# Kernel optimization log

Hardware: AMD Instinct MI355X
Metric: run time of the kernel (lower is better)

Reference implementation:

```python
import jax, jax.numpy as jnp
import numpy as np

# Graph / model dims (match init_kwargs config)
N1, N2, N3 = 80000, 16000, 4096
E1, E2 = 256000, 65536
D_IN, H1, C1 = 256, 8, 64   # conv1: concat -> 512
H2, C2 = 4, 64              # conv2: mean over heads -> gnn_outdim=64
F_IN, F_HID, L_DIM, N_CLS = 128, 64, 64, 1


def setup_inputs() -> dict:
    key = jax.random.key(0)
    ks = jax.random.split(key, 20)
    rng = np.random.default_rng(0)

    def edges(E, n_src, n_dst):
        src = rng.integers(0, n_src, size=E)
        dst = rng.integers(0, n_dst, size=E)
        # avoid incidental self loops (PyG remove_self_loops); explicit ones added in conv
        src = np.where(src == dst, src + 1, src)
        return jnp.asarray(src, jnp.int32), jnp.asarray(dst, jnp.int32)

    es1, ed1 = edges(E1, N1, N2)
    es2, ed2 = edges(E2, N2, N3)
    s = 0.05
    return {
        "x": jax.random.normal(ks[0], (N1, D_IN), jnp.float32),
        "flat": jax.random.normal(ks[1], (N3, F_IN), jnp.float32),
        "last": jax.random.normal(ks[2], (N3, L_DIM), jnp.float32),
        "edge_src1": es1, "edge_dst1": ed1,
        "edge_src2": es2, "edge_dst2": ed2,
        "W1_src": jax.random.normal(ks[3], (D_IN, H1 * C1), jnp.float32) * s,
        "W1_dst": jax.random.normal(ks[4], (D_IN, H1 * C1), jnp.float32) * s,
        "att1_src": jax.random.normal(ks[5], (H1, C1), jnp.float32) * s,
        "att1_dst": jax.random.normal(ks[6], (H1, C1), jnp.float32) * s,
        "bias1": jax.random.normal(ks[7], (H1 * C1,), jnp.float32) * s,
        "W2_src": jax.random.normal(ks[8], (H1 * C1, H2 * C2), jnp.float32) * s,
        "W2_dst": jax.random.normal(ks[9], (H1 * C1, H2 * C2), jnp.float32) * s,
        "att2_src": jax.random.normal(ks[10], (H2, C2), jnp.float32) * s,
        "att2_dst": jax.random.normal(ks[11], (H2, C2), jnp.float32) * s,
        "bias2": jax.random.normal(ks[12], (C2,), jnp.float32) * s,
        "flat_W": jax.random.normal(ks[13], (F_IN, F_HID), jnp.float32) * s,
        "flat_b": jax.random.normal(ks[14], (F_HID,), jnp.float32) * s,
        "out_W": jax.random.normal(ks[15], (C2 + F_HID + L_DIM, N_CLS), jnp.float32) * s,
        "out_b": jax.random.normal(ks[16], (N_CLS,), jnp.float32) * s,
    }


def gat_conv(x_src, x_dst, src, dst, W_s, W_d, a_s, a_d, b, concat):
    """PyG bipartite GATConv (eval mode, add_self_loops=True, neg slope 0.2)."""
    H, C = a_s.shape
    Ns, Nd = x_src.shape[0], x_dst.shape[0]
    h_s = (x_src @ W_s).reshape(Ns, H, C)
    h_d = (x_dst @ W_d).reshape(Nd, H, C)
    sl = jnp.arange(Nd, dtype=src.dtype)
    src = jnp.concatenate([src, sl])  # self loops on target nodes
    dst = jnp.concatenate([dst, sl])
    e_s = jnp.einsum("nhc,hc->nh", h_s, a_s)  # [Ns,H]
    e_d = jnp.einsum("nhc,hc->nh", h_d, a_d)  # [Nd,H]
    alpha = jax.nn.leaky_relu(e_s[src] + e_d[dst], negative_slope=0.2)  # [E,H]
    amax = jax.ops.segment_max(alpha, dst, num_segments=Nd)[dst]
    ex = jnp.exp(alpha - amax)
    w = ex / jax.ops.segment_sum(ex, dst, num_segments=Nd)[dst]  # segment softmax
    msg = w[:, :, None] * h_s[src]  # [E,H,C]
    out = jax.ops.segment_sum(msg, dst, num_segments=Nd)  # [Nd,H,C]
    out = out.reshape(Nd, H * C) if concat else out.mean(axis=1)
    return out + b


def reference(x, flat, last, edge_src1, edge_dst1, edge_src2, edge_dst2,
              W1_src, W1_dst, att1_src, att1_dst, bias1,
              W2_src, W2_dst, att2_src, att2_dst, bias2,
              flat_W, flat_b, out_W, out_b):
    # eval mode: featdrop / attndrop / main_dropout are identity
    h = gat_conv(x, x[:N2], edge_src1, edge_dst1,
                 W1_src, W1_dst, att1_src, att1_dst, bias1, concat=True)
    h = jax.nn.elu(h)
    h = gat_conv(h, h[:N3], edge_src2, edge_dst2,
                 W2_src, W2_dst, att2_src, att2_dst, bias2, concat=False)
    f = flat @ flat_W + flat_b
    z = jnp.concatenate([h, f, last], axis=1)  # [N3, 64+64+64]
    return z @ out_W + out_b  # [N3, num_cls]
```

## Files before the change

### kernel.cpp

```cpp
#include <hip/hip_runtime.h>
#include <hip/hip_bf16.h>
#include <cstdio>

typedef __attribute__((ext_vector_type(8))) short short8;
typedef __attribute__((ext_vector_type(4))) short short4v;
typedef __attribute__((ext_vector_type(8))) _Float16 half8;
typedef __attribute__((ext_vector_type(4))) float f32x4;

template <int H> struct VecT;
template <> struct VecT<8> { using T = short8; };
template <> struct VecT<4> { using T = short4v; };

__device__ __forceinline__ float bfu2f(unsigned short u) {
    return __uint_as_float(((unsigned)u) << 16);
}
__device__ __forceinline__ unsigned short f2bfu(float f) {
    __hip_bfloat16 b = __float2bfloat16(f);
    union { __hip_bfloat16 b; unsigned short u; } cv; cv.b = b;
    return cv.u;
}
__device__ __forceinline__ unsigned short f2hu(float f) {
    _Float16 h = (_Float16)f;
    union { _Float16 h; unsigned short u; } cv; cv.h = h;
    return cv.u;
}

#define N1 80000
#define N2 16000
#define N3 4096
#define E1 256000
#define E2 65536

__global__ void prep_kernel(const float* __restrict__ W1s, unsigned short* __restrict__ w1s_pk,
                            const float* __restrict__ W2s, unsigned short* __restrict__ w2s_pk,
                            const float* __restrict__ W1d, const float* __restrict__ a1d,
                            float* __restrict__ v1dT,
                            const float* __restrict__ W2d, const float* __restrict__ a2d,
                            float* __restrict__ v2dT,
                            const float* __restrict__ fW, unsigned short* __restrict__ fw_t3,
                            int* __restrict__ zbase, int zn) {
    int i = blockIdx.x * blockDim.x + threadIdx.x;
    const int S0 = 131072, S1 = 131072, S2 = 8192, S3 = 4096;
    if (i < S0) {
        int k = i >> 9, n = i & 511;
        int n16 = n >> 4, l = n & 15, k32 = k >> 5, qq = (k >> 3) & 3, e = k & 7;
        size_t base = ((size_t)(n16 * 8 + k32)) * 512 + (qq * 16 + l) * 8 + e;
        w1s_pk[base] = f2hu(W1s[i]);
    } else if (i < S0 + S1) {
        int j = i - S0;
        int k = j >> 8, n = j & 255;
        int n16 = n >> 4, l = n & 15, k32 = k >> 5, qq = (k >> 3) & 3, e = k & 7;
        size_t base = ((size_t)(n16 * 16 + k32)) * 512 + (qq * 16 + l) * 8 + e;
        w2s_pk[base] = f2hu(W2s[j]);
    } else if (i < S0 + S1 + S2) {
        int j = i - S0 - S1;
        int k = j >> 6, n = j & 63;
        float v = fW[j];
        unsigned short h = f2bfu(v);
        unsigned short l = f2bfu(v - bfu2f(h));
        size_t base = (size_t)n * 384;
        fw_t3[base + k] = h;
        fw_t3[base + 128 + k] = l;
        fw_t3[base + 256 + k] = h;
    } else if (i < S0 + S1 + S2 + S3) {
        int j = i - S0 - S1 - S2;
        if (j < 2048) {
            int h = j >> 8, k = j & 255;
            float s = 0.f;
            for (int c = 0; c < 64; c++) s += W1d[k * 512 + h * 64 + c] * a1d[h * 64 + c];
            v1dT[j] = s;
        } else {
            int jj = j - 2048;
            int h = jj >> 9, k = jj & 511;
            float s = 0.f;
            for (int c = 0; c < 64; c++) s += W2d[k * 256 + h * 64 + c] * a2d[h * 64 + c];
            v2dT[jj] = s;
        }
    } else {
        int j = i - S0 - S1 - S2 - S3;
        if (j < zn) zbase[j] = 0;
    }
}

__global__ void hist_dual(const int* __restrict__ d1, int* __restrict__ c1,
                          const int* __restrict__ d2, int* __restrict__ c2) {
    int i = blockIdx.x * blockDim.x + threadIdx.x;
    if (i < E1) {
        int d = d1[i];
        if ((unsigned)d < (unsigned)N2) atomicAdd(&c1[d], 1);
    } else if (i < E1 + E2) {
        int d = d2[i - E1];
        if ((unsigned)d < (unsigned)N3) atomicAdd(&c2[d], 1);
    }
}
__global__ __launch_bounds__(1024)
void scan_dual(const int* __restrict__ c1, int* __restrict__ s1, int Nd1,
               const int* __restrict__ c2, int* __restrict__ s2, int Nd2) {
    const int* cnt = (blockIdx.x == 0) ? c1 : c2;
    int* start = (blockIdx.x == 0) ? s1 : s2;
    int Nd = (blockIdx.x == 0) ? Nd1 : Nd2;
    __shared__ int part[1024];
    int t = threadIdx.x;
    int k = (Nd + 1023) >> 10;
    int lo = t * k, hi = min(lo + k, Nd);
    if (lo > Nd) lo = Nd;
    int s = 0;
    for (int i = lo; i < hi; i++) s += cnt[i];
    part[t] = s;
    __syncthreads();
    for (int off = 1; off < 1024; off <<= 1) {
        int v = (t >= off) ? part[t - off] : 0;
        __syncthreads();
        part[t] += v;
        __syncthreads();
    }
    int run = (t > 0) ? part[t - 1] : 0;
    for (int i = lo; i < hi; i++) { start[i] = run; run += cnt[i]; }
    if (t == 1023) start[Nd] = part[1023];
}
__global__ void fill_dual(const int* __restrict__ sa1, const int* __restrict__ da1,
                          const int* __restrict__ st1, int* __restrict__ cu1, int* __restrict__ cs1,
                          const int* __restrict__ sa2, const int* __restrict__ da2,
                          const int* __restrict__ st2, int* __restrict__ cu2, int* __restrict__ cs2) {
    int i = blockIdx.x * blockDim.x + threadIdx.x;
    const int *sa, *da, *st;
    int *cu, *cs;
    int Nd, Ns, e;
    if (i < E1) { sa = sa1; da = da1; st = st1; cu = cu1; cs = cs1; Nd = N2; Ns = N1; e = i; }
    else if (i < E1 + E2) { sa = sa2; da = da2; st = st2; cu = cu2; cs = cs2; Nd = N3; Ns = N2; e = i - E1; }
    else return;
    int d = da[e];
    if ((unsigned)d >= (unsigned)Nd) return;
    int p = atomicAdd(&cu[d], 1);
    int idx = st[d] + p;
    if (idx >= st[d + 1]) return;
    int s = sa[e];
    if ((unsigned)s >= (unsigned)Ns) s = 0;
    cs[idx] = s;
}

template <bool AF16>
__global__ __launch_bounds__(256, 2)
void gemm_lds(const void* __restrict__ Ax,
              const unsigned short* __restrict__ Bp, unsigned short* __restrict__ C,
              const float* __restrict__ att, float* __restrict__ es_out,
              int MT, int NB, int N, int K, int H) {
    __shared__ alignas(16) _Float16 As[2][64][72];
    const int hb = blockIdx.x;
    const int xcd = hb & 7;
    const int sI = hb >> 3;
    const int mt = (sI / NB) * 8 + xcd;
    const int nb = sI % NB;
    if (mt >= MT) return;
    const int m0 = mt * 64;
    const int tid = threadIdx.x;
    const int wave = tid >> 6, lane = tid & 63;
    const int q = lane >> 4, l15 = lane & 15;
    const int n0 = nb * 256 + wave * 64;
    const int KS = K >> 6;
    const int KSB = K >> 5;
    const int arow = tid >> 2, ac16 = (tid & 3) * 16;
    const unsigned short* Bbase = Bp + (size_t)(n0 >> 4) * KSB * 512 + lane * 8;

    f32x4 acc[4][4] = {};
    half8 b[2][4];
    float4 s0, s1, s2, s3;
    half8 sh0, sh1;

    auto stageLoad = [&](int t) {
        if constexpr (AF16) {
            const _Float16* p = (const _Float16*)Ax + (size_t)(m0 + arow) * K + t * 64 + ac16;
            sh0 = *(const half8*)p;
            sh1 = *(const half8*)(p + 8);
        } else {
            const float* p = (const float*)Ax + (size_t)(m0 + arow) * K + t * 64 + ac16;
            s0 = *(const float4*)p;
            s1 = *(const float4*)(p + 4);
            s2 = *(const float4*)(p + 8);
            s3 = *(const float4*)(p + 12);
        }
    };
    auto stageWrite = [&](int buf) {
        half8 v0, v1;
        if constexpr (AF16) {
            v0 = sh0; v1 = sh1;
        } else {
            v0[0] = (_Float16)s0.x; v0[1] = (_Float16)s0.y;
            v0[2] = (_Float16)s0.z; v0[3] = (_Float16)s0.w;
            v0[4] = (_Float16)s1.x; v0[5] = (_Float16)s1.y;
            v0[6] = (_Float16)s1.z; v0[7] = (_Float16)s1.w;
            v1[0] = (_Float16)s2.x; v1[1] = (_Float16)s2.y;
            v1[2] = (_Float16)s2.z; v1[3] = (_Float16)s2.w;
            v1[4] = (_Float16)s3.x; v1[5] = (_Float16)s3.y;
            v1[6] = (_Float16)s3.z; v1[7] = (_Float16)s3.w;
        }
        *(half8*)&As[buf][arow][ac16] = v0;
        *(half8*)&As[buf][arow][ac16 + 8] = v1;
    };
    auto loadB = [&](int k32, int kh, int nt) {
        b[kh][nt] = *(const half8*)(Bbase + ((size_t)nt * KSB + k32) * 512);
    };

    stageLoad(0);
#pragma unroll
    for (int kh = 0; kh < 2; kh++)
#pragma unroll
        for (int nt = 0; nt < 4; nt++) loadB(kh, kh, nt);
    stageWrite(0);
    __syncthreads();

    int cur = 0;
    for (int t = 0; t < KS; t++) {
        const bool hn = (t + 1) < KS;
        if (hn) stageLoad(t + 1);
#pragma unroll
        for (int kh = 0; kh < 2; kh++) {
#pragma unroll
            for (int rg = 0; rg < 4; rg++) {
                half8 a = *(const half8*)&As[cur][rg * 16 + l15][kh * 32 + q * 8];
#pragma unroll
                for (int nt = 0; nt < 4; nt++) {
                    acc[rg][nt] = __builtin_amdgcn_mfma_f32_16x16x32_f16(a, b[kh][nt], acc[rg][nt], 0, 0, 0);
                    if (rg == 3 && hn) loadB(2 * (t + 1) + kh, kh, nt);
                }
            }
        }
        if (hn) {
            stageWrite(cur ^ 1);
            __syncthreads();
        }
        cur ^= 1;
    }

#pragma unroll
    for (int rg = 0; rg < 4; rg++)
#pragma unroll
        for (int nt = 0; nt < 4; nt++)
#pragma unroll
            for (int r = 0; r < 4; r++) {
                int row = m0 + rg * 16 + q * 4 + r;
                int col = n0 + nt * 16 + l15;
                C[(size_t)row * N + col] = f2bfu(acc[rg][nt][r]);
            }
    {
        const int head = n0 >> 6;
        float av[4];
#pragma unroll
        for (int nt = 0; nt < 4; nt++) av[nt] = att[head * 64 + nt * 16 + l15];
#pragma unroll
        for (int rg = 0; rg < 4; rg++)
#pragma unroll
            for (int r = 0; r < 4; r++) {
                float p = acc[rg][0][r] * av[0] + acc[rg][1][r] * av[1]
                        + acc[rg][2][r] * av[2] + acc[rg][3][r] * av[3];
#pragma unroll
                for (int off = 1; off < 16; off <<= 1) p += __shfl_xor(p, off);
                if (l15 == 0)
                    es_out[(size_t)(m0 + rg * 16 + q * 4 + r) * H + head] = p;
            }
    }
}

__global__ __launch_bounds__(256)
void gemm_mfma(const float* __restrict__ A, const unsigned short* __restrict__ Bt3,
               float* __restrict__ C, int M, int N, int K) {
    const int KK = 3 * K;
    __shared__ unsigned short As[2][64][72];
    __shared__ unsigned short Bs[64][72];
    const int tid = threadIdx.x;
    const int wave = tid >> 6, lane = tid & 63;
    const int wr = wave >> 1, wc = wave & 1;
    const int quad = lane >> 4, l15 = lane & 15;
    const int m0 = blockIdx.y * 64, n0 = blockIdx.x * 64;
    f32x4 acc[2][2] = {};
    for (int k0 = 0; k0 < KK; k0 += 64) {
        const int seg = k0 / K;
        const int ks = k0 - seg * K;
#pragma unroll
        for (int i = 0; i < 2; i++) {
            int idx = tid + i * 256;
            int r = idx >> 3, cv = (idx & 7) * 8;
            const float* ap = &A[(size_t)(m0 + r) * K + ks + cv];
            const float4 v0 = *(const float4*)ap;
            const float4 v1 = *(const float4*)(ap + 4);
            float va[8] = {v0.x, v0.y, v0.z, v0.w, v1.x, v1.y, v1.z, v1.w};
            short8 h8, l8;
#pragma unroll
            for (int j = 0; j < 8; j++) {
                unsigned short hh = f2bfu(va[j]);
                h8[j] = (short)hh;
                l8[j] = (short)f2bfu(va[j] - bfu2f(hh));
            }
            *(short8*)&As[0][r][cv] = h8;
            *(short8*)&As[1][r][cv] = l8;
            *(short8*)&Bs[r][cv] = *(const short8*)&Bt3[(size_t)(n0 + r) * KK + k0 + cv];
        }
        __syncthreads();
        const int abank = (seg < 2) ? 0 : 1;
#pragma unroll
        for (int kk = 0; kk < 64; kk += 32) {
            short8 a[2], b[2];
#pragma unroll
            for (int t = 0; t < 2; t++) {
                a[t] = *(const short8*)&As[abank][wr * 32 + t * 16 + l15][kk + quad * 8];
                b[t] = *(const short8*)&Bs[wc * 32 + t * 16 + l15][kk + quad * 8];
            }
#pragma unroll
            for (int mt = 0; mt < 2; mt++)
#pragma unroll
                for (int nt = 0; nt < 2; nt++)
                    acc[mt][nt] = __builtin_amdgcn_mfma_f32_16x16x32_bf16(
                        a[mt], b[nt], acc[mt][nt], 0, 0, 0);
        }
        __syncthreads();
    }
#pragma unroll
    for (int mt = 0; mt < 2; mt++)
#pragma unroll
        for (int nt = 0; nt < 2; nt++)
#pragma unroll
            for (int r = 0; r < 4; r++) {
                int row = m0 + wr * 32 + mt * 16 + quad * 4 + r;
                int col = n0 + wc * 32 + nt * 16 + l15;
                C[(size_t)row * N + col] = acc[mt][nt][r];
            }
}

template <int H, bool ELU, bool HOUT, bool XF16, int KD>
__global__ __launch_bounds__(256)
void gat_agg2(const int* __restrict__ csr, const int* __restrict__ rs,
              const unsigned short* __restrict__ hs,
              const float* __restrict__ es,
              const void* __restrict__ xsrc,
              const float* __restrict__ vdT,
              const float* __restrict__ bias,
              void* __restrict__ out,
              int Nd) {
    constexpr int LH = (H == 8) ? 3 : 2;
    constexpr int EPC = 64 >> LH;
    constexpr int KPL = KD / EPC;
    const int lane = threadIdx.x & 63;
    const int d = blockIdx.x * (blockDim.x >> 6) + (threadIdx.x >> 6);
    if (d >= Nd) return;
    const int h = lane & (H - 1);
    const int e0 = lane >> LH;
    float edh = 0.f;
    {
        const float* vp = vdT + h * KD + e0 * KPL;
        if constexpr (XF16) {
            const _Float16* xr = (const _Float16*)xsrc + (size_t)d * KD + e0 * KPL;
#pragma unroll
            for (int i8 = 0; i8 < KPL / 8; i8++) {
                half8 hx = *(const half8*)(xr + i8 * 8);
#pragma unroll
                for (int jj = 0; jj < 8; jj++) edh += (float)hx[jj] * vp[i8 * 8 + jj];
            }
        } else {
            const float* xr = (const float*)xsrc + (size_t)d * KD + e0 * KPL;
#pragma unroll
            for (int i4 = 0; i4 < KPL / 4; i4++) {
                float4 xv = *(const float4*)(xr + i4 * 4);
                float4 vv = *(const float4*)(vp + i4 * 4);
                edh += xv.x * vv.x + xv.y * vv.y + xv.z * vv.z + xv.w * vv.w;
            }
        }
#pragma unroll
        for (int off = H; off < 64; off <<= 1) edh += __shfl_xor(edh, off);
    }
    const int beg = rs[d];
    const int deg = rs[d + 1] - beg;
    const int n = deg + 1;
    const int nch = (n + EPC - 1) / EPC;
    const int hB = lane >> (6 - LH);
    using V = typename VecT<H>::T;
    float acc[H] = {};
    const size_t rowoff = (size_t)lane * H;
    if (nch <= 8) {
        float ac[8];
        float mx = -1e30f;
#pragma unroll
        for (int c = 0; c < 8; c++) {
            float a = -1e30f;
            if (c < nch) {
                int j = c * EPC + e0;
                if (j < n) {
                    int s = (j < deg) ? csr[beg + j] : d;
                    a = es[(size_t)s * H + h] + edh;
                    a = (a > 0.0f) ? a : 0.2f * a;
                }
            }
            ac[c] = a;
            mx = fmaxf(mx, a);
        }
#pragma unroll
        for (int off = H; off < 64; off <<= 1) mx = fmaxf(mx, __shfl_xor(mx, off));
        float den = 0.0f;
#pragma unroll
        for (int c = 0; c < 8; c++)
            if (c < nch) den += expf(ac[c] - mx);
#pragma unroll
        for (int off = H; off < 64; off <<= 1) den += __shfl_xor(den, off);
        const float inv = 1.0f / den;
        float ec[8];
#pragma unroll
        for (int c = 0; c < 8; c++) ec[c] = expf(ac[c] - mx) * inv;
#pragma unroll
        for (int c = 0; c < 8; c++) {
            if (c >= nch) break;
            const int jb = c * EPC;
            const int cnt = min(EPC, n - jb);
            int s[EPC]; V rv[EPC];
#pragma unroll
            for (int u = 0; u < EPC; u++)
                if (u < cnt) { int jj = jb + u; s[u] = (jj < deg) ? csr[beg + jj] : d; }
#pragma unroll
            for (int u = 0; u < EPC; u++)
                if (u < cnt) rv[u] = *(const V*)&hs[(size_t)s[u] * (H * 64) + rowoff];
#pragma unroll
            for (int u = 0; u < EPC; u++)
                if (u < cnt) {
                    float w = __shfl(ec[c], u * H + hB);
#pragma unroll
                    for (int k = 0; k < H; k++) acc[k] += w * bfu2f((unsigned short)rv[u][k]);
                }
        }
    } else {
        float mx = -1e30f;
        for (int j0 = 0; j0 < n; j0 += EPC) {
            int j = j0 + e0;
            if (j < n) {
                int s = (j < deg) ? csr[beg + j] : d;
                float a = es[(size_t)s * H + h] + edh;
                a = (a > 0.0f) ? a : 0.2f * a;
                mx = fmaxf(mx, a);
            }
        }
#pragma unroll
        for (int off = H; off < 64; off <<= 1) mx = fmaxf(mx, __shfl_xor(mx, off));
        float den = 0.0f;
        for (int j0 = 0; j0 < n; j0 += EPC) {
            int j = j0 + e0;
            if (j < n) {
                int s = (j < deg) ? csr[beg + j] : d;
                float a = es[(size_t)s * H + h] + edh;
                a = (a > 0.0f) ? a : 0.2f * a;
                den += expf(a - mx);
            }
        }
#pragma unroll
        for (int off = H; off < 64; off <<= 1) den += __shfl_xor(den, off);
        const float inv = 1.0f / den;
        const float mB = __shfl(mx, hB);
        const float invB = __shfl(inv, hB);
        const float edhB = __shfl(edh, hB);
        int j = 0;
        for (; j + 4 <= n; j += 4) {
            int s[4]; V rv[4]; float w[4];
#pragma unroll
            for (int u = 0; u < 4; u++) { int jj = j + u; s[u] = (jj < deg) ? csr[beg + jj] : d; }
#pragma unroll
            for (int u = 0; u < 4; u++) rv[u] = *(const V*)&hs[(size_t)s[u] * (H * 64) + rowoff];
#pragma unroll
            for (int u = 0; u < 4; u++) {
                float a = es[(size_t)s[u] * H + hB] + edhB;
                a = (a > 0.0f) ? a : 0.2f * a;
                w[u] = expf(a - mB) * invB;
            }
#pragma unroll
            for (int u = 0; u < 4; u++)
#pragma unroll
                for (int k = 0; k < H; k++) acc[k] += w[u] * bfu2f((unsigned short)rv[u][k]);
        }
        for (; j < n; j++) {
            int s = (j < deg) ? csr[beg + j] : d;
            V rv = *(const V*)&hs[(size_t)s * (H * 64) + rowoff];
            float a = es[(size_t)s * H + hB] + edhB;
            a = (a > 0.0f) ? a : 0.2f * a;
            float w = expf(a - mB) * invB;
#pragma unroll
            for (int k = 0; k < H; k++) acc[k] += w * bfu2f((unsigned short)rv[k]);
        }
    }
#pragma unroll
    for (int k = 0; k < H; k++) {
        float v = acc[k];
        if (ELU) {
            v += bias[lane * H + k];
            v = (v > 0.0f) ? v : expm1f(v);
        }
        acc[k] = v;
    }
    if constexpr (HOUT) {
        half8 hv;
#pragma unroll
        for (int k = 0; k < H; k++) hv[k] = (_Float16)acc[k];
        _Float16* op = (_Float16*)out + (size_t)d * (H * 64) + rowoff;
        *(half8*)op = hv;
    } else {
        float* op = (float*)out + (size_t)d * (H * 64) + rowoff;
#pragma unroll
        for (int qd = 0; qd < H / 4; qd++)
            *(float4*)&op[qd * 4] = *(float4*)&acc[qd * 4];
    }
}

__global__ void final_kernel(const float* __restrict__ acc2, const float* __restrict__ bias2,
                             const float* __restrict__ fbuf, const float* __restrict__ flat_b,
                             const float* __restrict__ last, const float* __restrict__ outW,
                             const float* __restrict__ outb, float* __restrict__ out, int N) {
    int n = blockIdx.x * blockDim.x + threadIdx.x;
    if (n >= N) return;
    float s = outb[0];
    const float* a = acc2 + (size_t)n * 256;
    for (int c = 0; c < 64; c++) {
        float h2 = 0.25f * (a[c] + a[64 + c] + a[128 + c] + a[192 + c]) + bias2[c];
        s += h2 * outW[c];
        s += (fbuf[(size_t)n * 64 + c] + flat_b[c]) * outW[64 + c];
        s += last[(size_t)n * 64 + c] * outW[128 + c];
    }
    out[n] = s;
}

extern "C" void kernel_launch(void* const* d_in, const int* in_sizes, int n_in,
                              void* d_out, int out_size, void* d_ws, size_t ws_size,
                              hipStream_t stream) {
    const float* x    = (const float*)d_in[0];
    const float* flat = (const float*)d_in[1];
    const float* last = (const float*)d_in[2];
    const int*  es1i  = (const int*)d_in[3];
    const int*  ed1i  = (const int*)d_in[4];
    const int*  es2i  = (const int*)d_in[5];
    const int*  ed2i  = (const int*)d_in[6];
    const float* W1s  = (const float*)d_in[7];
    const float* W1d  = (const float*)d_in[8];
    const float* a1s  = (const float*)d_in[9];
    const float* a1d  = (const float*)d_in[10];
    const float* b1   = (const float*)d_in[11];
    const float* W2s  = (const float*)d_in[12];
    const float* W2d  = (const float*)d_in[13];
    const float* a2s  = (const float*)d_in[14];
    const float* a2d  = (const float*)d_in[15];
    const float* b2   = (const float*)d_in[16];
    const float* fW   = (const float*)d_in[17];
    const float* fb   = (const float*)d_in[18];
    const float* oW   = (const float*)d_in[19];
    const float* ob   = (const float*)d_in[20];
    float* out = (float*)d_out;

    float* ws = (float*)d_ws;
    unsigned short* hs1_bf = (unsigned short*)ws;
    float* es1f = ws + 24576000;
    float* acc1 = ws + 25344000;
    unsigned short* wb = (unsigned short*)(ws + 54016000);
    unsigned short* w1s_pk = wb;
    unsigned short* w2s_pk = wb + 524288;
    unsigned short* fw_t3  = wb + 1048576;
    float* v1dT = ws + 54600000;
    float* v2dT = ws + 54602048;
    int* ibase   = (int*)(ws + 54816000);
    int* cnt1    = ibase;
    int* cursor1 = ibase + 16000;
    int* cnt2    = ibase + 32000;
    int* cursor2 = ibase + 36096;
    int* start1  = ibase + 40192;
    int* start2  = ibase + 56193;
    int* csr1    = ibase + 60290;
    int* csr2    = ibase + 316290;
    const size_t NEED = ((size_t)54816000 + 381826) * 4;
    if (ws_size < NEED) {
        fprintf(stderr, "kernel_launch: ws_size %zu < needed %zu\n", ws_size, NEED);
        return;
    }
    unsigned short* hs2_bf = (unsigned short*)ws;
    float* es2f = ws + 2572288;
    float* acc2 = ws + 2652672;
    float* fbuf = ws + 3701248;
    unsigned short* acc1h = (unsigned short*)acc1;

    {
        int total = 131072 + 131072 + 8192 + 4096 + 40192;
        prep_kernel<<<(total + 255) / 256, 256, 0, stream>>>(
            W1s, w1s_pk, W2s, w2s_pk,
            W1d, a1d, v1dT, W2d, a2d, v2dT,
            fW, fw_t3, ibase, 40192);
    }
    hist_dual<<<(E1 + E2 + 255) / 256, 256, 0, stream>>>(ed1i, cnt1, ed2i, cnt2);
    scan_dual<<<2, 1024, 0, stream>>>(cnt1, start1, N2, cnt2, start2, N3);
    fill_dual<<<(E1 + E2 + 255) / 256, 256, 0, stream>>>(
        es1i, ed1i, start1, cursor1, csr1, es2i, ed2i, start2, cursor2, csr2);

    {
        const int MT = N1 / 64;
        const int NB = 2;
        const int grid = 8 * NB * ((MT + 7) / 8);
        gemm_lds<false><<<grid, 256, 0, stream>>>(
            x, w1s_pk, hs1_bf, a1s, es1f, MT, NB, 512, 256, 8);
    }
    gat_agg2<8, true, true, false, 256><<<N2 / 4, 256, 0, stream>>>(
        csr1, start1, hs1_bf, es1f, x, v1dT, b1, acc1h, N2);

    {
        const int MT = N2 / 64;
        const int grid = 8 * ((MT + 7) / 8);
        gemm_lds<true><<<grid, 256, 0, stream>>>(
            acc1h, w2s_pk, hs2_bf, a2s, es2f, MT, 1, 256, 512, 4);
    }
    gat_agg2<4, false, false, true, 512><<<N3 / 4, 256, 0, stream>>>(
        csr2, start2, hs2_bf, es2f, acc1h, v2dT, nullptr, acc2, N3);

    gemm_mfma<<<dim3(1, N3 / 64), 256, 0, stream>>>(flat, fw_t3, fbuf, N3, 64, 128);
    final_kernel<<<(N3 + 255) / 256, 256, 0, stream>>>(acc2, b2, fbuf, fb, last, oW, ob, out, N3);
}
```

Baseline: 385.0 us.

## Fuse flat GEMM into layer-2 GEMM launch and final head into aggregation

The flat-feature GEMM now runs as extra blocks inside the layer-2 projection GEMM launch, sharing one shared-memory buffer. The final linear head (head mean, bias, flat and last contributions, output dot) is folded into the layer-2 GAT aggregation epilogue using wave shuffles, so the acc2 intermediate and the final kernel go away. Two launches and a global round trip are removed. The edge-gather loop also drops its per-edge count guards and loads padded slots unconditionally, which simplifies control flow but may issue redundant loads.

```diff
diff --git a/kernel.cpp b/kernel.cpp
--- a/kernel.cpp
+++ b/kernel.cpp
@@ -140,13 +140,11 @@
 }
 
 template <bool AF16>
-__global__ __launch_bounds__(256, 2)
-void gemm_lds(const void* __restrict__ Ax,
+__device__ __forceinline__ void gemm_core(_Float16 (*As)[64][72],
+              const void* __restrict__ Ax,
               const unsigned short* __restrict__ Bp, unsigned short* __restrict__ C,
               const float* __restrict__ att, float* __restrict__ es_out,
-              int MT, int NB, int N, int K, int H) {
-    __shared__ alignas(16) _Float16 As[2][64][72];
-    const int hb = blockIdx.x;
+              int MT, int NB, int N, int K, int H, int hb) {
     const int xcd = hb & 7;
     const int sI = hb >> 3;
     const int mt = (sI / NB) * 8 + xcd;
@@ -261,17 +259,26 @@
     }
 }
 
-__global__ __launch_bounds__(256)
-void gemm_mfma(const float* __restrict__ A, const unsigned short* __restrict__ Bt3,
-               float* __restrict__ C, int M, int N, int K) {
-    const int KK = 3 * K;
-    __shared__ unsigned short As[2][64][72];
-    __shared__ unsigned short Bs[64][72];
+__global__ __launch_bounds__(256, 2)
+void gemm_l1(const void* __restrict__ Ax,
+             const unsigned short* __restrict__ Bp, unsigned short* __restrict__ C,
+             const float* __restrict__ att, float* __restrict__ es_out,
+             int MT, int NB, int N, int K, int H) {
+    __shared__ alignas(16) _Float16 As[2][64][72];
+    gemm_core<false>(As, Ax, Bp, C, att, es_out, MT, NB, N, K, H, blockIdx.x);
+}
+
+__device__ __forceinline__ void flat_core(unsigned char* smemraw,
+        const float* __restrict__ A, const unsigned short* __restrict__ Bt3,
+        float* __restrict__ C, int mb) {
+    const int K = 128, N = 64, KK = 384;
+    auto As = (unsigned short (*)[64][72])smemraw;
+    auto Bs = (unsigned short (*)[72])(smemraw + 18432);
     const int tid = threadIdx.x;
     const int wave = tid >> 6, lane = tid & 63;
     const int wr = wave >> 1, wc = wave & 1;
     const int quad = lane >> 4, l15 = lane & 15;
-    const int m0 = blockIdx.y * 64, n0 = blockIdx.x * 64;
+    const int m0 = mb * 64, n0 = 0;
     f32x4 acc[2][2] = {};
     for (int k0 = 0; k0 < KK; k0 += 64) {
         const int seg = k0 / K;
@@ -326,7 +333,23 @@
             }
 }
 
-template <int H, bool ELU, bool HOUT, bool XF16, int KD>
+__global__ __launch_bounds__(256, 2)
+void gemm2_flat(const void* __restrict__ Ax,
+                const unsigned short* __restrict__ Bp, unsigned short* __restrict__ C,
+                const float* __restrict__ att, float* __restrict__ es_out,
+                int MT, int NB, int N, int K, int H, int G2,
+                const float* __restrict__ fA, const unsigned short* __restrict__ fBt3,
+                float* __restrict__ fC) {
+    __shared__ alignas(16) unsigned char smem[27648];
+    if ((int)blockIdx.x < G2) {
+        gemm_core<true>((_Float16(*)[64][72])smem, Ax, Bp, C, att, es_out,
+                        MT, NB, N, K, H, blockIdx.x);
+    } else {
+        flat_core(smem, fA, fBt3, fC, blockIdx.x - G2);
+    }
+}
+
+template <int H, bool ELU, bool HOUT, bool XF16, int KD, bool FIN>
 __global__ __launch_bounds__(256)
 void gat_agg2(const int* __restrict__ csr, const int* __restrict__ rs,
               const unsigned short* __restrict__ hs,
@@ -335,7 +358,10 @@
               const float* __restrict__ vdT,
               const float* __restrict__ bias,
               void* __restrict__ out,
-              int Nd) {
+              int Nd,
+              const float* __restrict__ fbuf, const float* __restrict__ flat_b,
+              const float* __restrict__ last, const float* __restrict__ outW,
+              const float* __restrict__ outb, float* __restrict__ fout) {
     constexpr int LH = (H == 8) ? 3 : 2;
     constexpr int EPC = 64 >> LH;
     constexpr int KPL = KD / EPC;
@@ -408,21 +434,21 @@
         for (int c = 0; c < 8; c++) {
             if (c >= nch) break;
             const int jb = c * EPC;
-            const int cnt = min(EPC, n - jb);
             int s[EPC]; V rv[EPC];
 #pragma unroll
+            for (int u = 0; u < EPC; u++) {
+                int jj = jb + u;
+                s[u] = (jj < deg) ? csr[beg + jj] : d;
+            }
+#pragma unroll
             for (int u = 0; u < EPC; u++)
-                if (u < cnt) { int jj = jb + u; s[u] = (jj < deg) ? csr[beg + jj] : d; }
-#pragma unroll
-            for (int u = 0; u < EPC; u++)
-                if (u < cnt) rv[u] = *(const V*)&hs[(size_t)s[u] * (H * 64) + rowoff];
-#pragma unroll
-            for (int u = 0; u < EPC; u++)
-                if (u < cnt) {
-                    float w = __shfl(ec[c], u * H + hB);
-#pragma unroll
-                    for (int k = 0; k < H; k++) acc[k] += w * bfu2f((unsigned short)rv[u][k]);
-                }
+                rv[u] = *(const V*)&hs[(size_t)s[u] * (H * 64) + rowoff];
+#pragma unroll
+            for (int u = 0; u < EPC; u++) {
+                float w = __shfl(ec[c], u * H + hB);
+#pragma unroll
+                for (int k = 0; k < H; k++) acc[k] += w * bfu2f((unsigned short)rv[u][k]);
+            }
         }
     } else {
         float mx = -1e30f;
@@ -481,44 +507,55 @@
             for (int k = 0; k < H; k++) acc[k] += w * bfu2f((unsigned short)rv[k]);
         }
     }
-#pragma unroll
-    for (int k = 0; k < H; k++) {
-        float v = acc[k];
-        if (ELU) {
-            v += bias[lane * H + k];
-            v = (v > 0.0f) ? v : expm1f(v);
-        }
-        acc[k] = v;
-    }
-    if constexpr (HOUT) {
-        half8 hv;
-#pragma unroll
-        for (int k = 0; k < H; k++) hv[k] = (_Float16)acc[k];
-        _Float16* op = (_Float16*)out + (size_t)d * (H * 64) + rowoff;
-        *(half8*)op = hv;
+    if constexpr (FIN) {
+        float f4[4];
+#pragma unroll
+        for (int k = 0; k < 4; k++) {
+            float a2v = acc[k] + __shfl_xor(acc[k], 32);
+            f4[k] = a2v + __shfl_xor(a2v, 16);
+        }
+        float part = 0.f;
+        if (lane < 16) {
+            const int c0 = lane * 4;
+            float4 fb4 = *(const float4*)&fbuf[(size_t)d * 64 + c0];
+            float4 lb4 = *(const float4*)&last[(size_t)d * 64 + c0];
+            const float* fbv = &fb4.x;
+            const float* lbv = &lb4.x;
+#pragma unroll
+            for (int k = 0; k < 4; k++) {
+                int c = c0 + k;
+                float h2 = 0.25f * f4[k] + bias[c];
+                part += h2 * outW[c];
+                part += (fbv[k] + flat_b[c]) * outW[64 + c];
+                part += lbv[k] * outW[128 + c];
+            }
+        }
+#pragma unroll
+        for (int off = 1; off < 16; off <<= 1) part += __shfl_xor(part, off);
+        if (lane == 0) fout[d] = part + outb[0];
     } else {
-        float* op = (float*)out + (size_t)d * (H * 64) + rowoff;
-#pragma unroll
-        for (int qd = 0; qd < H / 4; qd++)
-            *(float4*)&op[qd * 4] = *(float4*)&acc[qd * 4];
-    }
-}
-
-__global__ void final_kernel(const float* __restrict__ acc2, const float* __restrict__ bias2,
-                             const float* __restrict__ fbuf, const float* __restrict__ flat_b,
-                             const float* __restrict__ last, const float* __restrict__ outW,
-                             const float* __restrict__ outb, float* __restrict__ out, int N) {
-    int n = blockIdx.x * blockDim.x + threadIdx.x;
-    if (n >= N) return;
-    float s = outb[0];
-    const float* a = acc2 + (size_t)n * 256;
-    for (int c = 0; c < 64; c++) {
-        float h2 = 0.25f * (a[c] + a[64 + c] + a[128 + c] + a[192 + c]) + bias2[c];
-        s += h2 * outW[c];
-        s += (fbuf[(size_t)n * 64 + c] + flat_b[c]) * outW[64 + c];
-        s += last[(size_t)n * 64 + c] * outW[128 + c];
-    }
-    out[n] = s;
+#pragma unroll
+        for (int k = 0; k < H; k++) {
+            float v = acc[k];
+            if (ELU) {
+                v += bias[lane * H + k];
+                v = (v > 0.0f) ? v : expm1f(v);
+            }
+            acc[k] = v;
+        }
+        if constexpr (HOUT) {
+            half8 hv;
+#pragma unroll
+            for (int k = 0; k < H; k++) hv[k] = (_Float16)acc[k];
+            _Float16* op = (_Float16*)out + (size_t)d * (H * 64) + rowoff;
+            *(half8*)op = hv;
+        } else {
+            float* op = (float*)out + (size_t)d * (H * 64) + rowoff;
+#pragma unroll
+            for (int qd = 0; qd < H / 4; qd++)
+                *(float4*)&op[qd * 4] = *(float4*)&acc[qd * 4];
+        }
+    }
 }
 
 extern "C" void kernel_launch(void* const* d_in, const int* in_sizes, int n_in,
@@ -573,7 +610,6 @@
     }
     unsigned short* hs2_bf = (unsigned short*)ws;
     float* es2f = ws + 2572288;
-    float* acc2 = ws + 2652672;
     float* fbuf = ws + 3701248;
     unsigned short* acc1h = (unsigned short*)acc1;
 
@@ -593,21 +629,21 @@
         const int MT = N1 / 64;
         const int NB = 2;
         const int grid = 8 * NB * ((MT + 7) / 8);
-        gemm_lds<false><<<grid, 256, 0, stream>>>(
+        gemm_l1<<<grid, 256, 0, stream>>>(
             x, w1s_pk, hs1_bf, a1s, es1f, MT, NB, 512, 256, 8);
     }
-    gat_agg2<8, true, true, false, 256><<<N2 / 4, 256, 0, stream>>>(
-        csr1, start1, hs1_bf, es1f, x, v1dT, b1, acc1h, N2);
+    gat_agg2<8, true, true, false, 256, false><<<N2 / 4, 256, 0, stream>>>(
+        csr1, start1, hs1_bf, es1f, x, v1dT, b1, acc1h, N2,
+        nullptr, nullptr, nullptr, nullptr, nullptr, nullptr);
 
     {
         const int MT = N2 / 64;
-        const int grid = 8 * ((MT + 7) / 8);
-        gemm_lds<true><<<grid, 256, 0, stream>>>(
-            acc1h, w2s_pk, hs2_bf, a2s, es2f, MT, 1, 256, 512, 4);
-    }
-    gat_agg2<4, false, false, true, 512><<<N3 / 4, 256, 0, stream>>>(
-        csr2, start2, hs2_bf, es2f, acc1h, v2dT, nullptr, acc2, N3);
-
-    gemm_mfma<<<dim3(1, N3 / 64), 256, 0, stream>>>(flat, fw_t3, fbuf, N3, 64, 128);
-    final_kernel<<<(N3 + 255) / 256, 256, 0, stream>>>(acc2, b2, fbuf, fb, last, oW, ob, out, N3);
-}
+        const int G2 = 8 * ((MT + 7) / 8);
+        gemm2_flat<<<G2 + N3 / 64, 256, 0, stream>>>(
+            acc1h, w2s_pk, hs2_bf, a2s, es2f, MT, 1, 256, 512, 4, G2,
+            flat, fw_t3, fbuf);
+    }
+    gat_agg2<4, false, false, true, 512, true><<<N3 / 4, 256, 0, stream>>>(
+        csr2, start2, hs2_bf, es2f, acc1h, v2dT, b2, nullptr, N3,
+        fbuf, fb, last, oW, ob, out);
+}
```

Measured after the change: 350.7 us. 8.9% less time.
